# Kernel tuning notes

Measured on AMD Instinct MI355X. Metric: run time of the kernel, lower is better.

The kernel has to match this reference:

```python
import jax, jax.numpy as jnp
import numpy as np


def setup_inputs() -> dict:
    return {"n_nodes": 64, "seq_len": 128}


def reference(n_nodes, seq_len) -> jnp.ndarray:
    # Original torch code: zeros(n,n); block-diagonal ones; strict upper
    # triangle set to 1; diagonal set to 0; then transpose.
    # Equivalent closed form after the transpose:
    #   M[i,j] = 1 iff (i > j OR i//n_nodes == j//n_nodes) AND i != j
    n = seq_len * n_nodes
    idx = jnp.arange(n)
    i = idx[:, None]   # row index  [n,1]
    j = idx[None, :]   # col index  [1,n]
    same_block = (i // n_nodes) == (j // n_nodes)
    mask = ((i > j) | same_block) & (i != j)
    return mask.astype(jnp.float32)
```

## Files before the change

### kernel.cpp

```cpp
#include <hip/hip_runtime.h>
#include <math.h>


typedef float vfloat4 __attribute__((ext_vector_type(4)));

__global__ void __launch_bounds__(256)
Create_Mask_23871428231714_kernel(const int* __restrict__ n_nodes_p,
                                  float* __restrict__ out, int n) {
    const int i = blockIdx.x;
    const int n_nodes = *n_nodes_p;
    const int blk_end = (i / n_nodes + 1) * n_nodes;

    vfloat4* __restrict__ row = reinterpret_cast<vfloat4*>(out + (size_t)i * (size_t)n);
    const int nv = n >> 2;

    for (int v = threadIdx.x; v < nv; v += blockDim.x) {
        const int j0 = v << 2;
        vfloat4 val;
        val.x = ((j0     < blk_end) && (j0     != i)) ? 1.0f : 0.0f;
        val.y = ((j0 + 1 < blk_end) && (j0 + 1 != i)) ? 1.0f : 0.0f;
        val.z = ((j0 + 2 < blk_end) && (j0 + 2 != i)) ? 1.0f : 0.0f;
        val.w = ((j0 + 3 < blk_end) && (j0 + 3 != i)) ? 1.0f : 0.0f;
        __builtin_nontemporal_store(val, row + v);
    }
}

extern "C" void kernel_launch(void* const* d_in, const int* in_sizes, int n_in,
                              void* d_out, int out_size, void* d_ws, size_t ws_size,
                              hipStream_t stream) {
    (void)in_sizes; (void)n_in; (void)d_ws; (void)ws_size;
    const int* n_nodes_p = (const int*)d_in[0];
    float* out = (float*)d_out;

    const int n = (int)llround(sqrt((double)out_size));

    Create_Mask_23871428231714_kernel<<<dim3(n, 1, 1), dim3(256, 1, 1), 0, stream>>>(
        n_nodes_p, out, n);
}
```

Measured before the change: 264.2 us.

## Switch mask kernel to flat grid-stride loop with fixed grid

New measurement: 276.1 us. 4.5% more time.

```diff
diff --git a/kernel.cpp b/kernel.cpp
--- a/kernel.cpp
+++ b/kernel.cpp
@@ -6,22 +6,35 @@
 
 __global__ void __launch_bounds__(256)
 Create_Mask_23871428231714_kernel(const int* __restrict__ n_nodes_p,
-                                  float* __restrict__ out, int n) {
-    const int i = blockIdx.x;
+                                  float* __restrict__ out,
+                                  int n, int log2n) {
     const int n_nodes = *n_nodes_p;
-    const int blk_end = (i / n_nodes + 1) * n_nodes;
+    const bool nn_pow2 = (n_nodes & (n_nodes - 1)) == 0;
+    const int s = nn_pow2 ? (__ffs(n_nodes) - 1) : 0;
 
-    vfloat4* __restrict__ row = reinterpret_cast<vfloat4*>(out + (size_t)i * (size_t)n);
-    const int nv = n >> 2;
+    const size_t nv = ((size_t)n * (size_t)n) >> 2;
+    const size_t stride = (size_t)gridDim.x * blockDim.x;
+    vfloat4* __restrict__ o = reinterpret_cast<vfloat4*>(out);
 
-    for (int v = threadIdx.x; v < nv; v += blockDim.x) {
-        const int j0 = v << 2;
+    for (size_t idx = (size_t)blockIdx.x * blockDim.x + threadIdx.x;
+         idx < nv; idx += stride) {
+        const size_t flat = idx << 2;
+        int i, j0;
+        if (log2n >= 0) {
+            i  = (int)(flat >> log2n);
+            j0 = (int)(flat & (size_t)(n - 1));
+        } else {
+            i  = (int)(flat / (size_t)n);
+            j0 = (int)(flat - (size_t)i * (size_t)n);
+        }
+        const int blk_end = nn_pow2 ? (((i >> s) + 1) << s)
+                                    : ((i / n_nodes + 1) * n_nodes);
         vfloat4 val;
         val.x = ((j0     < blk_end) && (j0     != i)) ? 1.0f : 0.0f;
         val.y = ((j0 + 1 < blk_end) && (j0 + 1 != i)) ? 1.0f : 0.0f;
         val.z = ((j0 + 2 < blk_end) && (j0 + 2 != i)) ? 1.0f : 0.0f;
         val.w = ((j0 + 3 < blk_end) && (j0 + 3 != i)) ? 1.0f : 0.0f;
-        __builtin_nontemporal_store(val, row + v);
+        __builtin_nontemporal_store(val, o + idx);
     }
 }
 
@@ -33,7 +46,10 @@
     float* out = (float*)d_out;
 
     const int n = (int)llround(sqrt((double)out_size));
+    int log2n = -1;
+    if ((n & (n - 1)) == 0) { log2n = 0; while ((1 << log2n) < n) ++log2n; }
 
-    Create_Mask_23871428231714_kernel<<<dim3(n, 1, 1), dim3(256, 1, 1), 0, stream>>>(
-        n_nodes_p, out, n);
+    const int grid = 2048;
+    Create_Mask_23871428231714_kernel<<<dim3(grid, 1, 1), dim3(256, 1, 1), 0, stream>>>(
+        n_nodes_p, out, n, log2n);
 }
```
